# Kernel tuning notes

Hardware: AMD Instinct MI355X
Metric: run time of the kernel (lower is better)

The kernel has to match this reference:

```python
import jax, jax.numpy as jnp
import numpy as np

ALPHA = 0.2  # LeakyReLU negative slope
NEG_INF = -9e15

def setup_inputs() -> dict:
    key = jax.random.key(0)
    k1, k2, k3, k4 = jax.random.split(key, 4)
    N, IN_F, OUT_F = 12288, 256, 128
    h = jax.random.normal(k1, (N, IN_F), dtype=jnp.float32)
    adj = jax.random.randint(k2, (N, N), 0, 2, dtype=jnp.int32)
    # Xavier-uniform-like init with gain 1.414
    limW = 1.414 * np.sqrt(6.0 / (IN_F + OUT_F))
    W = jax.random.uniform(k3, (IN_F, OUT_F), dtype=jnp.float32, minval=-limW, maxval=limW)
    lima = 1.414 * np.sqrt(6.0 / (2 * OUT_F + 1))
    a = jax.random.uniform(k4, (2 * OUT_F, 1), dtype=jnp.float32, minval=-lima, maxval=lima)
    return {"h": h, "adj": adj, "W": W, "a": a}

def reference(h, adj, W, a):
    out_f = W.shape[1]
    Wh = h @ W                      # [N, out_f]
    Wh1 = Wh @ a[:out_f, :]         # [N, 1]
    Wh2 = Wh @ a[out_f:, :]         # [N, 1]
    e = Wh1 + Wh2.T                 # [N, N] broadcast-add scores
    e = jnp.where(e > 0, e, ALPHA * e)  # LeakyReLU
    scores = jnp.where(adj > 0, e, NEG_INF)
    attention = jax.nn.softmax(scores, axis=1)  # dropout is identity at inference
    h_prime = attention @ Wh        # [N, out_f]
    return jax.nn.elu(h_prime)      # concat=True -> ELU
```

## Files before the change

### kernel.cpp

```cpp
#include <hip/hip_runtime.h>

#define NN   12288
#define FIN  256
#define FOUT 128
#define ALPHA 0.2f

typedef __attribute__((ext_vector_type(8))) _Float16 half8v;
typedef __attribute__((ext_vector_type(4))) float float4v;
typedef __attribute__((ext_vector_type(4))) int   int4v;


__global__ __launch_bounds__(128) void k_wh(
    const float* __restrict__ h,
    const float* __restrict__ W,
    const float* __restrict__ a,
    _Float16* __restrict__ WhT2,
    float* __restrict__ Wh1, float* __restrict__ Wh2,
    float* __restrict__ mxArr)
{
    __shared__ float sP1[2][16], sP2[2][16];
    const int t = threadIdx.x;
    const int row0 = blockIdx.x * 16;

    float acc[16];
    #pragma unroll
    for (int r = 0; r < 16; ++r) acc[r] = 0.f;

    const float* hb = h + (size_t)row0 * FIN;
    for (int k = 0; k < FIN; k += 4) {
        const float w0 = W[(k + 0) * FOUT + t];
        const float w1 = W[(k + 1) * FOUT + t];
        const float w2 = W[(k + 2) * FOUT + t];
        const float w3 = W[(k + 3) * FOUT + t];
        #pragma unroll
        for (int r = 0; r < 16; ++r) {
            const float4v hv = *(const float4v*)(hb + r * FIN + k);
            float s = acc[r];
            s = fmaf(hv.x, w0, s);
            s = fmaf(hv.y, w1, s);
            s = fmaf(hv.z, w2, s);
            s = fmaf(hv.w, w3, s);
            acc[r] = s;
        }
    }

    half8v pk0, pk1;
    #pragma unroll
    for (int r = 0; r < 8; ++r)  pk0[r] = (_Float16)acc[r];
    #pragma unroll
    for (int r = 0; r < 8; ++r)  pk1[r] = (_Float16)acc[8 + r];
    _Float16* dst = WhT2 + (size_t)(row0 >> 5) * 4096 + t * 32 + (row0 & 16);
    *(half8v*)(dst)     = pk0;
    *(half8v*)(dst + 8) = pk1;

    const float a1t = a[t];
    const float a2t = a[FOUT + t];
    const int lane = t & 63, wv = t >> 6;
    #pragma unroll
    for (int r = 0; r < 16; ++r) {
        float v1 = acc[r] * a1t;
        float v2 = acc[r] * a2t;
        #pragma unroll
        for (int off = 1; off < 64; off <<= 1) {
            v1 += __shfl_xor(v1, off, 64);
            v2 += __shfl_xor(v2, off, 64);
        }
        if (lane == 0) { sP1[wv][r] = v1; sP2[wv][r] = v2; }
    }
    __syncthreads();
    if (t < 16) {
        const float v1 = sP1[0][t] + sP1[1][t];
        float v2 = sP2[0][t] + sP2[1][t];
        Wh1[row0 + t] = v1;
        Wh2[row0 + t] = v2;
        #pragma unroll
        for (int off = 1; off < 16; off <<= 1)
            v2 = fmaxf(v2, __shfl_xor(v2, off, 64));
        if (t == 0) mxArr[blockIdx.x] = v2;
    }
}

static __device__ __forceinline__ half8v build_p(
    const int4v a0, const int4v a1, const float* wvv,
    const float wh1, const float M, float& S)
{
    const int av[8] = {a0.x, a0.y, a0.z, a0.w, a1.x, a1.y, a1.z, a1.w};
    half8v af;
    #pragma unroll
    for (int jj = 0; jj < 8; ++jj) {
        float e = wh1 + wvv[jj];
        e = fmaxf(e, ALPHA * e);
        const float p = av[jj] ? __expf(e - M) : 0.f;
        af[jj] = (_Float16)p;
        S += p;
    }
    return af;
}

static __device__ __forceinline__ float wave_gmax(
    const float* __restrict__ mxArr, int nmx, int lane)
{
    float mv = -1e30f;
    for (int idx = lane; idx < nmx; idx += 64) mv = fmaxf(mv, mxArr[idx]);
    #pragma unroll
    for (int off = 1; off < 64; off <<= 1)
        mv = fmaxf(mv, __shfl_xor(mv, off, 64));
    return mv;
}

__global__ __launch_bounds__(64, 2) void k_attn(
    const int* __restrict__ adj,
    const _Float16* __restrict__ WhT2,
    const float* __restrict__ Wh1, const float* __restrict__ Wh2,
    const float* __restrict__ mxArr, int nmx,
    float* __restrict__ pC, float* __restrict__ pS)
{
    const int lane = threadIdx.x;
    const int m    = lane & 15;
    const int q    = lane >> 4;
    const int rowbase = blockIdx.x * 64;
    const int J    = gridDim.y;
    const int jy   = blockIdx.y;
    const int jlen = NN / J;
    const int jbeg = jy * jlen;

    const float mxv = wave_gmax(mxArr, nmx, lane);

    float wh1[4], Mi[4];
    const int* rowp[4];
    #pragma unroll
    for (int rg = 0; rg < 4; ++rg) {
        const int row = rowbase + rg * 16 + m;
        wh1[rg] = Wh1[row];
        const float tm = wh1[rg] + mxv;
        Mi[rg] = fmaxf(tm, ALPHA * tm);
        rowp[rg] = adj + (size_t)row * NN;
    }

    float4v c[4][8];
    #pragma unroll
    for (int rg = 0; rg < 4; ++rg)
        #pragma unroll
        for (int t = 0; t < 8; ++t) c[rg][t] = (float4v){0.f, 0.f, 0.f, 0.f};
    float S[4] = {0.f, 0.f, 0.f, 0.f};

    for (int j0 = jbeg; j0 < jbeg + jlen; j0 += 32) {
        const int jb = j0 + q * 8;

        int4v a0[4], a1[4];
        #pragma unroll
        for (int rg = 0; rg < 4; ++rg) {
            a0[rg] = __builtin_nontemporal_load((const int4v*)(rowp[rg] + jb));
            a1[rg] = __builtin_nontemporal_load((const int4v*)(rowp[rg] + jb + 4));
        }
        const _Float16* tp = WhT2 + (size_t)(j0 >> 5) * 4096;
        half8v b[8];
        #pragma unroll
        for (int t = 0; t < 8; ++t)
            b[t] = *(const half8v*)(tp + (t * 16 + m) * 32 + q * 8);
        const float4v w0 = *(const float4v*)(Wh2 + jb);
        const float4v w1 = *(const float4v*)(Wh2 + jb + 4);
        const float wvv[8] = {w0.x, w0.y, w0.z, w0.w, w1.x, w1.y, w1.z, w1.w};

        #pragma unroll
        for (int rg = 0; rg < 4; ++rg) {
            const half8v af = build_p(a0[rg], a1[rg], wvv, wh1[rg], Mi[rg], S[rg]);
            #pragma unroll
            for (int t = 0; t < 8; ++t)
                c[rg][t] = __builtin_amdgcn_mfma_f32_16x16x32_f16(af, b[t], c[rg][t], 0, 0, 0);
        }
    }

    #pragma unroll
    for (int rg = 0; rg < 4; ++rg) {
        S[rg] += __shfl_xor(S[rg], 16, 64);
        S[rg] += __shfl_xor(S[rg], 32, 64);
        if (q == 0) pS[(size_t)jy * NN + rowbase + rg * 16 + m] = S[rg];
    }

    #pragma unroll
    for (int rg = 0; rg < 4; ++rg)
        #pragma unroll
        for (int t = 0; t < 8; ++t)
            #pragma unroll
            for (int reg = 0; reg < 4; ++reg) {
                const int row = rowbase + rg * 16 + q * 4 + reg;
                pC[((size_t)jy * NN + row) * FOUT + t * 16 + m] = c[rg][t][reg];
            }
}

__global__ __launch_bounds__(256) void k_reduce(
    const float* __restrict__ pC, const float* __restrict__ pS,
    float* __restrict__ out, int J)
{
    const int idx = blockIdx.x * 256 + threadIdx.x;
    const int row = idx >> 5;
    const int c4  = (idx & 31) * 4;
    float4v acc = (float4v){0.f, 0.f, 0.f, 0.f};
    float S = 0.f;
    for (int j = 0; j < J; ++j) {
        const float4v v = *(const float4v*)(pC + ((size_t)j * NN + row) * FOUT + c4);
        acc.x += v.x; acc.y += v.y; acc.z += v.z; acc.w += v.w;
        S += pS[(size_t)j * NN + row];
    }
    const float inv = 1.f / fmaxf(S, 1e-30f);
    float4v r;
    #pragma unroll
    for (int k = 0; k < 4; ++k) {
        const float v = acc[k] * inv;
        r[k] = (v > 0.f) ? v : (__expf(v) - 1.f);
    }
    *(float4v*)(out + (size_t)row * FOUT + c4) = r;
}

__global__ __launch_bounds__(64, 2) void k_attn_fb(
    const int* __restrict__ adj,
    const _Float16* __restrict__ WhT2,
    const float* __restrict__ Wh1, const float* __restrict__ Wh2,
    const float* __restrict__ mxArr, int nmx,
    float* __restrict__ out)
{
    const int lane = threadIdx.x;
    const int m    = lane & 15;
    const int q    = lane >> 4;
    const int rowbase = blockIdx.x * 64;

    const float mxv = wave_gmax(mxArr, nmx, lane);

    float wh1[4], Mi[4];
    const int* rowp[4];
    #pragma unroll
    for (int rg = 0; rg < 4; ++rg) {
        const int row = rowbase + rg * 16 + m;
        wh1[rg] = Wh1[row];
        const float tm = wh1[rg] + mxv;
        Mi[rg] = fmaxf(tm, ALPHA * tm);
        rowp[rg] = adj + (size_t)row * NN;
    }

    float4v c[4][8];
    #pragma unroll
    for (int rg = 0; rg < 4; ++rg)
        #pragma unroll
        for (int t = 0; t < 8; ++t) c[rg][t] = (float4v){0.f, 0.f, 0.f, 0.f};
    float S[4] = {0.f, 0.f, 0.f, 0.f};

    for (int j0 = 0; j0 < NN; j0 += 32) {
        const int jb = j0 + q * 8;
        int4v a0[4], a1[4];
        #pragma unroll
        for (int rg = 0; rg < 4; ++rg) {
            a0[rg] = __builtin_nontemporal_load((const int4v*)(rowp[rg] + jb));
            a1[rg] = __builtin_nontemporal_load((const int4v*)(rowp[rg] + jb + 4));
        }
        const _Float16* tp = WhT2 + (size_t)(j0 >> 5) * 4096;
        half8v b[8];
        #pragma unroll
        for (int t = 0; t < 8; ++t)
            b[t] = *(const half8v*)(tp + (t * 16 + m) * 32 + q * 8);
        const float4v w0 = *(const float4v*)(Wh2 + jb);
        const float4v w1 = *(const float4v*)(Wh2 + jb + 4);
        const float wvv[8] = {w0.x, w0.y, w0.z, w0.w, w1.x, w1.y, w1.z, w1.w};
        #pragma unroll
        for (int rg = 0; rg < 4; ++rg) {
            const half8v af = build_p(a0[rg], a1[rg], wvv, wh1[rg], Mi[rg], S[rg]);
            #pragma unroll
            for (int t = 0; t < 8; ++t)
                c[rg][t] = __builtin_amdgcn_mfma_f32_16x16x32_f16(af, b[t], c[rg][t], 0, 0, 0);
        }
    }

    #pragma unroll
    for (int rg = 0; rg < 4; ++rg) {
        S[rg] += __shfl_xor(S[rg], 16, 64);
        S[rg] += __shfl_xor(S[rg], 32, 64);
        #pragma unroll
        for (int reg = 0; reg < 4; ++reg) {
            const int mloc = q * 4 + reg;
            const float Sr = __shfl(S[rg], mloc, 64);
            const float inv = 1.f / fmaxf(Sr, 1e-30f);
            #pragma unroll
            for (int t = 0; t < 8; ++t) {
                const float v = c[rg][t][reg] * inv;
                out[(size_t)(rowbase + rg * 16 + mloc) * FOUT + t * 16 + m] =
                    (v > 0.f) ? v : (__expf(v) - 1.f);
            }
        }
    }
}

extern "C" void kernel_launch(void* const* d_in, const int* in_sizes, int n_in,
                              void* d_out, int out_size, void* d_ws, size_t ws_size,
                              hipStream_t stream) {
    const float* h   = (const float*)d_in[0];
    const int*   adj = (const int*)d_in[1];
    const float* W   = (const float*)d_in[2];
    const float* a   = (const float*)d_in[3];
    float* out = (float*)d_out;

    char* ws = (char*)d_ws;
    float* Wh1   = (float*)ws;
    float* Wh2   = (float*)(ws + 49152);
    float* mxArr = (float*)(ws + 98304);
    _Float16* WhT2 = (_Float16*)(ws + 101376);
    const size_t base_need = 101376ULL + 3145728ULL;
    const int NB = NN / 16;

    int J = 8;
    while (J > 1 &&
           base_need + (size_t)J * NN * 4 + (size_t)J * NN * FOUT * 4 > ws_size)
        J >>= 1;
    const bool ok =
        base_need + (size_t)NN * 4 + (size_t)NN * FOUT * 4 <= ws_size;

    k_wh<<<NB, 128, 0, stream>>>(h, W, a, WhT2, Wh1, Wh2, mxArr);
    if (ok) {
        float* pS = (float*)(ws + base_need);
        float* pC = pS + (size_t)J * NN;
        k_attn<<<dim3(NN / 64, J), 64, 0, stream>>>(adj, WhT2, Wh1, Wh2,
                                                    mxArr, NB, pC, pS);
        k_reduce<<<(NN * (FOUT / 4)) / 256, 256, 0, stream>>>(pC, pS, out, J);
    } else {
        k_attn_fb<<<NN / 64, 64, 0, stream>>>(adj, WhT2, Wh1, Wh2, mxArr, NB, out);
    }
}
```

Baseline: 1.016 ms.

## Halve rows per wave and software-prefetch next adj tile in attention kernel

```diff
diff --git a/kernel.cpp b/kernel.cpp
--- a/kernel.cpp
+++ b/kernel.cpp
@@ -118,7 +118,7 @@
     const int lane = threadIdx.x;
     const int m    = lane & 15;
     const int q    = lane >> 4;
-    const int rowbase = blockIdx.x * 64;
+    const int rowbase = blockIdx.x * 32;
     const int J    = gridDim.y;
     const int jy   = blockIdx.y;
     const int jlen = NN / J;
@@ -126,10 +126,10 @@
 
     const float mxv = wave_gmax(mxArr, nmx, lane);
 
-    float wh1[4], Mi[4];
-    const int* rowp[4];
-    #pragma unroll
-    for (int rg = 0; rg < 4; ++rg) {
+    float wh1[2], Mi[2];
+    const int* rowp[2];
+    #pragma unroll
+    for (int rg = 0; rg < 2; ++rg) {
         const int row = rowbase + rg * 16 + m;
         wh1[rg] = Wh1[row];
         const float tm = wh1[rg] + mxv;
@@ -137,33 +137,55 @@
         rowp[rg] = adj + (size_t)row * NN;
     }
 
-    float4v c[4][8];
-    #pragma unroll
-    for (int rg = 0; rg < 4; ++rg)
+    float4v c[2][8];
+    #pragma unroll
+    for (int rg = 0; rg < 2; ++rg)
         #pragma unroll
         for (int t = 0; t < 8; ++t) c[rg][t] = (float4v){0.f, 0.f, 0.f, 0.f};
-    float S[4] = {0.f, 0.f, 0.f, 0.f};
-
-    for (int j0 = jbeg; j0 < jbeg + jlen; j0 += 32) {
-        const int jb = j0 + q * 8;
-
-        int4v a0[4], a1[4];
-        #pragma unroll
-        for (int rg = 0; rg < 4; ++rg) {
-            a0[rg] = __builtin_nontemporal_load((const int4v*)(rowp[rg] + jb));
-            a1[rg] = __builtin_nontemporal_load((const int4v*)(rowp[rg] + jb + 4));
-        }
+    float S[2] = {0.f, 0.f};
+
+    int4v na0[2], na1[2];
+    float4v nw0, nw1;
+    {
+        const int jb = jbeg + q * 8;
+        #pragma unroll
+        for (int rg = 0; rg < 2; ++rg) {
+            na0[rg] = __builtin_nontemporal_load((const int4v*)(rowp[rg] + jb));
+            na1[rg] = __builtin_nontemporal_load((const int4v*)(rowp[rg] + jb + 4));
+        }
+        nw0 = *(const float4v*)(Wh2 + jb);
+        nw1 = *(const float4v*)(Wh2 + jb + 4);
+    }
+
+    const int iters = jlen / 32;
+    for (int it = 0; it < iters; ++it) {
+        const int j0 = jbeg + it * 32;
+
+        const int4v a0[2] = {na0[0], na0[1]};
+        const int4v a1[2] = {na1[0], na1[1]};
+        const float4v w0 = nw0, w1 = nw1;
+
+        if (it + 1 < iters) {
+            const int jb = j0 + 32 + q * 8;
+            #pragma unroll
+            for (int rg = 0; rg < 2; ++rg) {
+                na0[rg] = __builtin_nontemporal_load((const int4v*)(rowp[rg] + jb));
+                na1[rg] = __builtin_nontemporal_load((const int4v*)(rowp[rg] + jb + 4));
+            }
+            nw0 = *(const float4v*)(Wh2 + jb);
+            nw1 = *(const float4v*)(Wh2 + jb + 4);
+        }
+
         const _Float16* tp = WhT2 + (size_t)(j0 >> 5) * 4096;
         half8v b[8];
         #pragma unroll
         for (int t = 0; t < 8; ++t)
             b[t] = *(const half8v*)(tp + (t * 16 + m) * 32 + q * 8);
-        const float4v w0 = *(const float4v*)(Wh2 + jb);
-        const float4v w1 = *(const float4v*)(Wh2 + jb + 4);
+
         const float wvv[8] = {w0.x, w0.y, w0.z, w0.w, w1.x, w1.y, w1.z, w1.w};
 
         #pragma unroll
-        for (int rg = 0; rg < 4; ++rg) {
+        for (int rg = 0; rg < 2; ++rg) {
             const half8v af = build_p(a0[rg], a1[rg], wvv, wh1[rg], Mi[rg], S[rg]);
             #pragma unroll
             for (int t = 0; t < 8; ++t)
@@ -172,14 +194,14 @@
     }
 
     #pragma unroll
-    for (int rg = 0; rg < 4; ++rg) {
+    for (int rg = 0; rg < 2; ++rg) {
         S[rg] += __shfl_xor(S[rg], 16, 64);
         S[rg] += __shfl_xor(S[rg], 32, 64);
         if (q == 0) pS[(size_t)jy * NN + rowbase + rg * 16 + m] = S[rg];
     }
 
     #pragma unroll
-    for (int rg = 0; rg < 4; ++rg)
+    for (int rg = 0; rg < 2; ++rg)
         #pragma unroll
         for (int t = 0; t < 8; ++t)
             #pragma unroll
@@ -223,14 +245,14 @@
     const int lane = threadIdx.x;
     const int m    = lane & 15;
     const int q    = lane >> 4;
-    const int rowbase = blockIdx.x * 64;
+    const int rowbase = blockIdx.x * 32;
 
     const float mxv = wave_gmax(mxArr, nmx, lane);
 
-    float wh1[4], Mi[4];
-    const int* rowp[4];
-    #pragma unroll
-    for (int rg = 0; rg < 4; ++rg) {
+    float wh1[2], Mi[2];
+    const int* rowp[2];
+    #pragma unroll
+    for (int rg = 0; rg < 2; ++rg) {
         const int row = rowbase + rg * 16 + m;
         wh1[rg] = Wh1[row];
         const float tm = wh1[rg] + mxv;
@@ -238,18 +260,18 @@
         rowp[rg] = adj + (size_t)row * NN;
     }
 
-    float4v c[4][8];
-    #pragma unroll
-    for (int rg = 0; rg < 4; ++rg)
+    float4v c[2][8];
+    #pragma unroll
+    for (int rg = 0; rg < 2; ++rg)
         #pragma unroll
         for (int t = 0; t < 8; ++t) c[rg][t] = (float4v){0.f, 0.f, 0.f, 0.f};
-    float S[4] = {0.f, 0.f, 0.f, 0.f};
+    float S[2] = {0.f, 0.f};
 
     for (int j0 = 0; j0 < NN; j0 += 32) {
         const int jb = j0 + q * 8;
-        int4v a0[4], a1[4];
-        #pragma unroll
-        for (int rg = 0; rg < 4; ++rg) {
+        int4v a0[2], a1[2];
+        #pragma unroll
+        for (int rg = 0; rg < 2; ++rg) {
             a0[rg] = __builtin_nontemporal_load((const int4v*)(rowp[rg] + jb));
             a1[rg] = __builtin_nontemporal_load((const int4v*)(rowp[rg] + jb + 4));
         }
@@ -262,7 +284,7 @@
         const float4v w1 = *(const float4v*)(Wh2 + jb + 4);
         const float wvv[8] = {w0.x, w0.y, w0.z, w0.w, w1.x, w1.y, w1.z, w1.w};
         #pragma unroll
-        for (int rg = 0; rg < 4; ++rg) {
+        for (int rg = 0; rg < 2; ++rg) {
             const half8v af = build_p(a0[rg], a1[rg], wvv, wh1[rg], Mi[rg], S[rg]);
             #pragma unroll
             for (int t = 0; t < 8; ++t)
@@ -271,7 +293,7 @@
     }
 
     #pragma unroll
-    for (int rg = 0; rg < 4; ++rg) {
+    for (int rg = 0; rg < 2; ++rg) {
         S[rg] += __shfl_xor(S[rg], 16, 64);
         S[rg] += __shfl_xor(S[rg], 32, 64);
         #pragma unroll
@@ -317,10 +339,10 @@
     if (ok) {
         float* pS = (float*)(ws + base_need);
         float* pC = pS + (size_t)J * NN;
-        k_attn<<<dim3(NN / 64, J), 64, 0, stream>>>(adj, WhT2, Wh1, Wh2,
+        k_attn<<<dim3(NN / 32, J), 64, 0, stream>>>(adj, WhT2, Wh1, Wh2,
                                                     mxArr, NB, pC, pS);
         k_reduce<<<(NN * (FOUT / 4)) / 256, 256, 0, stream>>>(pC, pS, out, J);
     } else {
-        k_attn_fb<<<NN / 64, 64, 0, stream>>>(adj, WhT2, Wh1, Wh2, mxArr, NB, out);
-    }
-}
+        k_attn_fb<<<NN / 32, 64, 0, stream>>>(adj, WhT2, Wh1, Wh2, mxArr, NB, out);
+    }
+}
```

After: 930.7 us. 1.09x faster.
